# Kernel tuning notes

Measured on AMD Instinct MI355X. Metric: run time of the kernel, lower is better.

## Reference

```python
import jax, jax.numpy as jnp
import numpy as np

DN = ('NCHW', 'OIHW', 'NCHW')
LN_EPS = 1e-5
L2_EPS = 1e-12


def dwconv(x, w, pad):
    # depthwise conv: x [b,c,h,w], w [c,1,kh,kw]
    return jax.lax.conv_general_dilated(
        x, w, (1, 1), [(pad, pad), (pad, pad)],
        dimension_numbers=DN, feature_group_count=x.shape[1])


def l2norm(x):
    n = jnp.sqrt(jnp.sum(x * x, axis=-1, keepdims=True))
    return x / jnp.maximum(n, L2_EPS)


def setup_inputs() -> dict:
    key = jax.random.key(0)
    L, c, heads, mult = 2, 512, 8, 4
    cm = c * mult
    ks = jax.random.split(key, 18)
    rn = lambda k, s, sc=0.02: jax.random.normal(k, s, jnp.float32) * sc
    return {
        'x': jax.random.normal(ks[0], (2, c, 128, 128), jnp.float32),
        'Wq': rn(ks[1], (L, c, c)),
        'Wk': rn(ks[2], (L, c, c)),
        'Wv': rn(ks[3], (L, c, c)),
        'rescale': jnp.ones((L, heads, 1, 1), jnp.float32),
        'proj_W': rn(ks[4], (L, c, c)),
        'proj_b': jnp.zeros((L, c), jnp.float32),
        'pos_w1': rn(ks[5], (L, c, 1, 3, 3)),
        'pos_w2': rn(ks[6], (L, c, 1, 3, 3)),
        'ln_g': jnp.ones((L, c), jnp.float32),
        'ln_b': jnp.zeros((L, c), jnp.float32),
        'w1': rn(ks[7], (L, cm, c)),
        'dw1': rn(ks[8], (L, cm // 4, 1, 1, 1), 0.1),
        'dw3': rn(ks[9], (L, cm // 4, 1, 3, 3), 0.1),
        'dw5': rn(ks[10], (L, cm // 4, 1, 5, 5), 0.1),
        'dw7': rn(ks[11], (L, cm // 4, 1, 7, 7), 0.1),
        'w2': rn(ks[12], (L, c, cm)),
    }


def reference(x, Wq, Wk, Wv, rescale, proj_W, proj_b, pos_w1, pos_w2,
              ln_g, ln_b, w1, dw1, dw3, dw5, dw7, w2):
    b, c, H, W = x.shape
    heads = rescale.shape[1]
    d = c // heads
    n = H * W
    x = x.transpose(0, 2, 3, 1)  # [b,H,W,c]
    for l in range(Wq.shape[0]):
        # ---- S_MSA (channel-wise transposed attention) ----
        xf = x.reshape(b, n, c)
        q_inp = xf @ Wq[l]
        k_inp = xf @ Wk[l]
        v_inp = xf @ Wv[l]
        # [b,n,heads,d] -> [b,heads,d,n]
        to_hd = lambda t: t.reshape(b, n, heads, d).transpose(0, 2, 3, 1)
        q, k, v = to_hd(q_inp), to_hd(k_inp), to_hd(v_inp)
        q = l2norm(q)
        k = l2norm(k)
        attn = jnp.einsum('bhdn,bhen->bhde', k, q) * rescale[l]  # [b,h,d,d]
        attn = jax.nn.softmax(attn, axis=-1)
        o = jnp.einsum('bhde,bhen->bhdn', attn, v)
        o = o.transpose(0, 3, 1, 2).reshape(b, n, c)  # [b,n,heads*d]
        out_c = (o @ proj_W[l] + proj_b[l]).reshape(b, H, W, c)
        # positional branch on v_inp
        vimg = v_inp.reshape(b, H, W, c).transpose(0, 3, 1, 2)
        p = dwconv(vimg, pos_w1[l], 1)
        p = jax.nn.gelu(p, approximate=False)
        p = dwconv(p, pos_w2[l], 1)
        x = x + out_c + p.transpose(0, 2, 3, 1)
        # ---- PreNorm + MS_FFN ----
        mu = x.mean(-1, keepdims=True)
        var = jnp.mean((x - mu) ** 2, axis=-1, keepdims=True)
        xn = (x - mu) / jnp.sqrt(var + LN_EPS) * ln_g[l] + ln_b[l]
        y = xn.transpose(0, 3, 1, 2)  # [b,c,H,W]
        y = jnp.einsum('oc,bchw->bohw', w1[l], y)  # [b,4c,H,W]
        y1, y2, y3, y4 = jnp.split(y, 4, axis=1)
        o1 = dwconv(y1, dw1[l], 0)
        o2 = dwconv(y2, dw3[l], 1)
        o3 = dwconv(y3, dw5[l], 2)
        o4 = dwconv(y4, dw7[l], 3)
        o = jnp.concatenate([o1, o2, o3, o4], axis=1) + y
        o = jnp.einsum('oc,bchw->bohw', w2[l], o)  # [b,c,H,W]
        x = x + o.transpose(0, 2, 3, 1)
    return x.transpose(0, 3, 1, 2)
```

## Files before the change

### kernel.cpp

```cpp
#include <hip/hip_runtime.h>
#include <math.h>

typedef unsigned short u16;
typedef short bf16x8 __attribute__((ext_vector_type(8)));
typedef float f32x4 __attribute__((ext_vector_type(4)));
typedef float f32x2 __attribute__((ext_vector_type(2)));

__device__ __forceinline__ float bf2f(u16 h) {
    union { unsigned u; float f; } v; v.u = ((unsigned)h) << 16; return v.f;
}
__device__ __forceinline__ u16 f2bf(float f) {
    union { float f; unsigned u; } v; v.f = f;
    unsigned r = v.u + 0x7fffu + ((v.u >> 16) & 1u);
    return (u16)(r >> 16);
}
__device__ __forceinline__ f32x2 up2(unsigned u) {
    union { unsigned v; float f; } lo, hi;
    lo.v = u << 16; hi.v = u & 0xffff0000u;
    f32x2 r; r.x = lo.f; r.y = hi.f; return r;
}
__device__ __forceinline__ f32x2 unpk(unsigned u) { return up2(u); }
__device__ __forceinline__ f32x4 unpk(uint2 u) {
    f32x2 a = up2(u.x), b = up2(u.y);
    f32x4 r; r.x = a.x; r.y = a.y; r.z = b.x; r.w = b.y; return r;
}
__device__ __forceinline__ unsigned pkbf(f32x2 v) {
    return (unsigned)f2bf(v.x) | ((unsigned)f2bf(v.y) << 16);
}
__device__ __forceinline__ uint2 pkbf(f32x4 v) {
    uint2 r;
    r.x = (unsigned)f2bf(v.x) | ((unsigned)f2bf(v.y) << 16);
    r.y = (unsigned)f2bf(v.z) | ((unsigned)f2bf(v.w) << 16);
    return r;
}
__device__ __forceinline__ float gl(float v) {
    return 0.5f * v * (1.f + erff(v * 0.70710678118654752f));
}

__device__ __forceinline__ void gload_lds16(const u16* g, u16* l) {
    __builtin_amdgcn_global_load_lds(
        (const __attribute__((address_space(1))) void*)g,
        (__attribute__((address_space(3))) void*)l, 16, 0, 0);
}

template<int N> struct VecT;
template<> struct VecT<2> { typedef f32x2 T; typedef unsigned U; };
template<> struct VecT<4> { typedef f32x4 T; typedef uint2 U; };

#define CH    512
#define NPIX  16384
#define PTOT  32768
#define NHEAD 8

__global__ void transpose_k(const float* __restrict__ in, float* outF, u16* outB,
                            int R, int Cc, size_t ibs, size_t obs)
{
    __shared__ float tile[32][33];
    int z = blockIdx.z;
    const float* ip = in + (size_t)z * ibs;
    int c0 = blockIdx.x * 32, r0 = blockIdx.y * 32;
    int tx = threadIdx.x, ty = threadIdx.y;
#pragma unroll
    for (int j = 0; j < 4; j++)
        tile[ty + j * 8][tx] = ip[(size_t)(r0 + ty + j * 8) * Cc + c0 + tx];
    __syncthreads();
#pragma unroll
    for (int j = 0; j < 4; j++) {
        int orow = c0 + ty + j * 8, ocol = r0 + tx;
        float v = tile[tx][ty + j * 8];
        size_t o = (size_t)z * obs + (size_t)orow * R + ocol;
        if (outF) outF[o] = v;
        if (outB) outB[o] = f2bf(v);
    }
}

__global__ void transpose16_k(const u16* __restrict__ in, u16* __restrict__ out,
                              int R, int Cc, size_t ibs, size_t obs)
{
    __shared__ u16 tile[32][34];
    int z = blockIdx.z;
    const u16* ip = in + (size_t)z * ibs;
    int c0 = blockIdx.x * 32, r0 = blockIdx.y * 32;
    int tx = threadIdx.x, ty = threadIdx.y;
#pragma unroll
    for (int j = 0; j < 4; j++)
        tile[ty + j * 8][tx] = ip[(size_t)(r0 + ty + j * 8) * Cc + c0 + tx];
    __syncthreads();
#pragma unroll
    for (int j = 0; j < 4; j++)
        out[(size_t)z * obs + (size_t)(c0 + ty + j * 8) * R + r0 + tx] = tile[tx][ty + j * 8];
}

__global__ void cvt_bf16_k(const float* __restrict__ in, u16* __restrict__ out)
{
    size_t i = ((size_t)blockIdx.x * 256 + threadIdx.x) * 4;
    float4 v = *(const float4*)&in[i];
    uint2 st;
    st.x = (unsigned)f2bf(v.x) | ((unsigned)f2bf(v.y) << 16);
    st.y = (unsigned)f2bf(v.z) | ((unsigned)f2bf(v.w) << 16);
    *(uint2*)&out[i] = st;
}

__global__ void cvtw2_k(const float* __restrict__ in, const float* __restrict__ dw1,
                        u16* __restrict__ out)
{
    size_t i = ((size_t)blockIdx.x * 256 + threadIdx.x) * 4;
    int cp = (int)(i & 2047);
    int l = (int)(i >> 20);
    int src; bool ps = false;
    if (cp < 512)       src = 1024 + cp;
    else if (cp < 1024) src = 1536 + (cp - 512);
    else if (cp < 1536) { src = cp - 1024; ps = true; }
    else                src = 512 + (cp - 1536);
    float4 v = *(const float4*)&in[(i & ~(size_t)2047) + src];
    if (ps) {
        v.x *= 1.f + dw1[l * 512 + src];
        v.y *= 1.f + dw1[l * 512 + src + 1];
        v.z *= 1.f + dw1[l * 512 + src + 2];
        v.w *= 1.f + dw1[l * 512 + src + 3];
    }
    uint2 st;
    st.x = (unsigned)f2bf(v.x) | ((unsigned)f2bf(v.y) << 16);
    st.y = (unsigned)f2bf(v.z) | ((unsigned)f2bf(v.w) << 16);
    *(uint2*)&out[i] = st;
}

__global__ __launch_bounds__(512) void gemm5_k(
    const u16* __restrict__ A, const u16* __restrict__ Bw,
    int K, int ldb, int Nn, int rowsPerBatch, int bStride, int kChunk,
    const float* __restrict__ bias, const float* resid,
    float* outF, u16* outB, const u16* __restrict__ addB)
{
    __shared__ __attribute__((aligned(16))) u16 smem[6 * 4096];
    u16* Asb = smem;
    u16* Bsb = smem + 3 * 4096;
    int tid = threadIdx.x;

    int gx = gridDim.x;
    int nwg = gx * gridDim.y;
    int lin = blockIdx.y * gx + blockIdx.x;
    int swz = lin;
    if ((nwg & 7) == 0) swz = (lin & 7) * (nwg >> 3) + (lin >> 3);
    int bx = swz % gx, by = swz / gx;

    int rowBase = by * 128, colBase = bx * 128;
    const u16* Bp = Bw + (size_t)(rowBase / rowsPerBatch) * bStride;

    int kb = 0, ke = K;
    float* outFp = outF;
    if (kChunk) {
        kb = blockIdx.z * kChunk; ke = kb + kChunk;
        outFp = outF + (size_t)blockIdx.z * (size_t)gridDim.y * 128 * Nn;
    }

    f32x4 acc[4][2] = {};
    int lane = tid & 63, wave = tid >> 6;
    int wr = wave >> 2, wc = wave & 3;
    int lm = lane & 15, lk = lane >> 4;

    int row0 = tid >> 2;
    int kc   = ((tid ^ (tid >> 3)) & 3) * 8;
    int lb0  = (tid & ~63) * 8;

    const size_t aR0 = (size_t)(rowBase + row0) * K;
    const size_t bR0 = (size_t)(colBase + row0) * ldb;

    auto STAGE = [&](int bsel, int k0) {
        gload_lds16(&A [aR0 + k0 + kc], Asb + bsel * 4096 + lb0);
        gload_lds16(&Bp[bR0 + k0 + kc], Bsb + bsel * 4096 + lb0);
    };

    const int nsteps = (ke - kb) >> 5;
    STAGE(0, kb);
    STAGE(1, kb + 32);
    const int sl = (lk ^ ((lm >> 1) & 3)) * 8;

    for (int s = 0; s < nsteps; ++s) {
        asm volatile("s_waitcnt vmcnt(2)" ::: "memory");
        __builtin_amdgcn_s_barrier();
        __builtin_amdgcn_sched_barrier(0);
        int kpf = kb + ((s + 2 < nsteps) ? (s + 2) : (nsteps - 1)) * 32;
        STAGE((s + 2) % 3, kpf);

        const u16* Ab = Asb + (s % 3) * 4096;
        const u16* Bb = Bsb + (s % 3) * 4096;
        bf16x8 af[4], bfr[2];
#pragma unroll
        for (int mt = 0; mt < 4; mt++)
            af[mt] = *(const bf16x8*)&Ab[(wr * 64 + mt * 16 + lm) * 32 + sl];
#pragma unroll
        for (int nt = 0; nt < 2; nt++)
            bfr[nt] = *(const bf16x8*)&Bb[(wc * 32 + nt * 16 + lm) * 32 + sl];
        __builtin_amdgcn_s_setprio(1);
#pragma unroll
        for (int mt = 0; mt < 4; mt++)
#pragma unroll
            for (int nt = 0; nt < 2; nt++)
                acc[mt][nt] = __builtin_amdgcn_mfma_f32_16x16x32_bf16(
                    af[mt], bfr[nt], acc[mt][nt], 0, 0, 0);
        __builtin_amdgcn_s_setprio(0);
    }

    {
        float* smf = (float*)smem;
        constexpr int PADW = 132;
        const int erow = tid >> 5;
        const int ecol = (tid & 31) * 4;
        const int gcol = colBase + ecol;
        f32x4 bv = {};
        if (bias) {
            bv.x = bias[gcol];     bv.y = bias[gcol + 1];
            bv.z = bias[gcol + 2]; bv.w = bias[gcol + 3];
        }
        for (int hf = 0; hf < 4; ++hf) {
            if (hf == 0) {
                __syncthreads();
            } else {
                asm volatile("s_waitcnt lgkmcnt(0)" ::: "memory");
                __builtin_amdgcn_s_barrier();
            }
            if (wr == (hf >> 1)) {
                int mtb = (hf & 1) * 2;
#pragma unroll
                for (int m2 = 0; m2 < 2; m2++) {
#pragma unroll
                    for (int nt = 0; nt < 2; nt++) {
                        int lr = m2 * 16 + lk * 4;
                        int lc = wc * 32 + nt * 16 + lm;
#pragma unroll
                        for (int r = 0; r < 4; r++)
                            smf[(lr + r) * PADW + lc] = acc[mtb + m2][nt][r];
                    }
                }
            }
            int r0 = rowBase + hf * 32 + erow, r1 = r0 + 16;
            size_t o0 = (size_t)r0 * Nn + gcol, o1 = (size_t)r1 * Nn + gcol;
            f32x4 rv0 = {}, rv1 = {};
            uint2 av0 = {}, av1 = {};
            if (resid) { rv0 = *(const f32x4*)&resid[o0]; rv1 = *(const f32x4*)&resid[o1]; }
            if (addB)  { av0 = *(const uint2*)&addB[o0];  av1 = *(const uint2*)&addB[o1]; }
            asm volatile("s_waitcnt lgkmcnt(0)" ::: "memory");
            __builtin_amdgcn_s_barrier();
            f32x4 v0 = *(f32x4*)&smf[erow * PADW + ecol];
            f32x4 v1 = *(f32x4*)&smf[(erow + 16) * PADW + ecol];
            v0 += bv; v1 += bv;
            if (resid) { v0 += rv0; v1 += rv1; }
            if (addB)  { v0 += unpk(av0); v1 += unpk(av1); }
            if (outFp) { *(f32x4*)&outFp[o0] = v0; *(f32x4*)&outFp[o1] = v1; }
            if (outB) {
                uint2 p0 = pkbf(v0), p1 = pkbf(v1);
                *(uint2*)&outB[o0] = p0; *(uint2*)&outB[o1] = p1;
            }
        }
    }
}

template<int TM, int TN>
__global__ __launch_bounds__(256) void gemm_nt_k(
    const u16* __restrict__ A, const u16* __restrict__ Bw,
    int K, int ldb, int Nn, int rowsPerBatch, int bStride, int kChunk,
    const float* __restrict__ bias, const float* resid,
    float* outF, u16* outB, const u16* __restrict__ addB)
{
    constexpr int MT = TM / 32;
    constexpr int NT = TN / 32;
    constexpr int ABUF = TM * 32;
    constexpr int BBUF = TN * 32;
    __shared__ __attribute__((aligned(16))) u16 smem[2 * ABUF + 2 * BBUF];
    u16* Asb = smem;
    u16* Bsb = smem + 2 * ABUF;
    int tid = threadIdx.x;

    int gx = gridDim.x;
    int nwg = gx * gridDim.y;
    int lin = blockIdx.y * gx + blockIdx.x;
    int swz = lin;
    if ((nwg & 7) == 0) swz = (lin & 7) * (nwg >> 3) + (lin >> 3);
    int bx = swz % gx, by = swz / gx;

    int rowBase = by * TM, colBase = bx * TN;
    const u16* Bp = Bw + (size_t)(rowBase / rowsPerBatch) * bStride;

    int kb = 0, ke = K;
    float* outFp = outF;
    if (kChunk) {
        kb = blockIdx.z * kChunk; ke = kb + kChunk;
        outFp = outF + (size_t)blockIdx.z * (size_t)gridDim.y * TM * Nn;
    }

    f32x4 acc[MT][NT] = {};
    int lane = tid & 63, wave = tid >> 6;
    int wr = wave >> 1, wc = wave & 1;
    int lm = lane & 15, lk = lane >> 4;

    int row0 = tid >> 2;
    int kc   = ((tid ^ (tid >> 3)) & 3) * 8;
    int lb0  = (tid & ~63) * 8;

    const size_t aR0 = (size_t)(rowBase + row0) * K;
    const size_t bR0 = (size_t)(colBase + row0) * ldb;
    const size_t aR1 = (size_t)(rowBase + 64 + row0) * K;
    const size_t bR1 = (size_t)(colBase + 64 + row0) * ldb;

    auto STAGE = [&](int bsel, int k0) {
        gload_lds16(&A [aR0 + k0 + kc], Asb + bsel * ABUF + lb0);
        gload_lds16(&Bp[bR0 + k0 + kc], Bsb + bsel * BBUF + lb0);
        if constexpr (TM == 128)
            gload_lds16(&A [aR1 + k0 + kc], Asb + bsel * ABUF + lb0 + 2048);
        if constexpr (TN == 128)
            gload_lds16(&Bp[bR1 + k0 + kc], Bsb + bsel * BBUF + lb0 + 2048);
    };

    STAGE(0, kb);
    __syncthreads();
    int buf = 0;
    const int sl = (lk ^ ((lm >> 1) & 3)) * 8;

    for (int k0 = kb; k0 < ke; k0 += 32) {
        if (k0 + 32 < ke) STAGE(buf ^ 1, k0 + 32);
        const u16* Ab = Asb + buf * ABUF;
        const u16* Bb = Bsb + buf * BBUF;
        bf16x8 af[MT], bfr[NT];
#pragma unroll
        for (int mt = 0; mt < MT; mt++)
            af[mt] = *(const bf16x8*)&Ab[(wr * (TM / 2) + mt * 16 + lm) * 32 + sl];
#pragma unroll
        for (int nt = 0; nt < NT; nt++)
            bfr[nt] = *(const bf16x8*)&Bb[(wc * (TN / 2) + nt * 16 + lm) * 32 + sl];
#pragma unroll
        for (int mt = 0; mt < MT; mt++)
#pragma unroll
            for (int nt = 0; nt < NT; nt++)
                acc[mt][nt] = __builtin_amdgcn_mfma_f32_16x16x32_bf16(
                    af[mt], bfr[nt], acc[mt][nt], 0, 0, 0);
        __syncthreads();
        buf ^= 1;
    }

    {
        float* smf = (float*)smem;
        constexpr int PADW = TN + 4;
        constexpr int HALVES = TM / 32;
        constexpr int HPW = (MT / 2 > 0) ? MT / 2 : 1;
        const int erow = tid >> 5;
        const int ecol = (tid & 31) * 4;
        for (int hf = 0; hf < HALVES; ++hf) {
            __syncthreads();
            if (wr == hf / HPW) {
                int mtb = (hf % HPW) * 2;
#pragma unroll
                for (int m2 = 0; m2 < 2; m2++) {
#pragma unroll
                    for (int nt = 0; nt < NT; nt++) {
                        int lr = m2 * 16 + lk * 4;
                        int lc = wc * (TN / 2) + nt * 16 + lm;
#pragma unroll
                        for (int r = 0; r < 4; r++)
                            smf[(lr + r) * PADW + lc] = acc[mtb + m2][nt][r];
                    }
                }
            }
            __syncthreads();
#pragma unroll
            for (int p = 0; p < 4; p++) {
                int lrow = erow + p * 8;
                int grow = rowBase + hf * 32 + lrow;
                int gcol = colBase + ecol;
                f32x4 v = *(f32x4*)&smf[lrow * PADW + ecol];
                if (bias) {
                    v.x += bias[gcol];     v.y += bias[gcol + 1];
                    v.z += bias[gcol + 2]; v.w += bias[gcol + 3];
                }
                size_t o = (size_t)grow * Nn + gcol;
                if (resid) { f32x4 rv = *(const f32x4*)&resid[o]; v += rv; }
                if (addB)  { f32x4 av = unpk(*(const uint2*)&addB[o]); v += av; }
                if (outFp) *(f32x4*)&outFp[o] = v;
                if (outB) { uint2 pk = pkbf(v); *(uint2*)&outB[o] = pk; }
            }
        }
    }
}

__global__ void sreduce_k(const float* __restrict__ Sp, u16* __restrict__ Sbf)
{
    int i = blockIdx.x * 256 + threadIdx.x;
    float s = 0.f;
#pragma unroll
    for (int z = 0; z < 16; z++) s += Sp[(size_t)z * 524288 + i];
    Sbf[i] = f2bf(s);
}

__global__ void nrm_k(const float* __restrict__ Wqf, const float* __restrict__ Wkf,
                      const float* __restrict__ T12f,
                      float* __restrict__ QNI, float* __restrict__ KNI)
{
    int idx = blockIdx.x * 256 + threadIdx.x;
    int e = idx & 511, b = (idx >> 9) & 1, which = idx >> 10;
    const float* w = which ? Wkf : Wqf;
    const float* Tf = T12f + which * 512;
    float s = 0.f;
    for (int c = 0; c < 512; c++)
        s += w[c * 512 + e] * Tf[(size_t)(b * 512 + c) * 1024 + e];
    s = fmaxf(s, 0.f);
    float* outp = which ? KNI : QNI;
    outp[b * 512 + e] = 1.f / fmaxf(sqrtf(s), 1e-12f);
}

__global__ __launch_bounds__(256) void gsmall_k(
    const float* __restrict__ T2f, const float* __restrict__ Wq,
    const float* __restrict__ qinv, const float* __restrict__ kinv,
    const float* __restrict__ resc, float* __restrict__ att)
{
    __shared__ float t2l[64][64], wql[64][64];
    int t = threadIdx.x, h = blockIdx.x, b = blockIdx.y;
    const int eg = (t & 15) * 4;
    const int dg = (t >> 4) * 4;
    f32x4 acc[4] = {};
    for (int c0 = 0; c0 < 512; c0 += 64) {
        __syncthreads();
        for (int i = t; i < 4096; i += 256) {
            int cc = i >> 6, j = i & 63;
            t2l[cc][j] = T2f[(size_t)(b * 512 + c0 + cc) * 1024 + h * 64 + j];
            wql[cc][j] = Wq[(size_t)(c0 + cc) * 512 + h * 64 + j];
        }
        __syncthreads();
        for (int cc = 0; cc < 64; cc++) {
            f32x4 qv = *(f32x4*)&wql[cc][eg];
            f32x4 dv = *(f32x4*)&t2l[cc][dg];
            acc[0] += dv.x * qv;
            acc[1] += dv.y * qv;
            acc[2] += dv.z * qv;
            acc[3] += dv.w * qv;
        }
    }
    float rs = resc[h];
    f32x4 qn = *(const f32x4*)&qinv[b * 512 + h * 64 + eg];
    float* ap = att + (size_t)(b * 8 + h) * 4096;
#pragma unroll
    for (int dj = 0; dj < 4; dj++) {
        int d = dg + dj;
        float kn = kinv[b * 512 + h * 64 + d];
        f32x4 v = acc[dj] * kn;
        v = v * qn;
        v.x *= rs; v.y *= rs; v.z *= rs; v.w *= rs;
        float m = fmaxf(fmaxf(v.x, v.y), fmaxf(v.z, v.w));
        for (int off = 1; off <= 8; off <<= 1) m = fmaxf(m, __shfl_xor(m, off));
        f32x4 ev;
        ev.x = expf(v.x - m); ev.y = expf(v.y - m);
        ev.z = expf(v.z - m); ev.w = expf(v.w - m);
        float s = ev.x + ev.y + ev.z + ev.w;
        for (int off = 1; off <= 8; off <<= 1) s += __shfl_xor(s, off);
        f32x4 r;
        r.x = ev.x / s; r.y = ev.y / s; r.z = ev.z / s; r.w = ev.w / s;
        *(f32x4*)&ap[d * 64 + eg] = r;
    }
}

__global__ __launch_bounds__(256) void mbuild_k(const float* __restrict__ attn,
                                                const float* __restrict__ projW,
                                                u16* Mnt)
{
    __shared__ float at[64][64];
    __shared__ float pw[64][64];
    int t = threadIdx.x;
    int h = blockIdx.x, b = blockIdx.y, ot = blockIdx.z;
    const float* ap = attn + (size_t)(b * NHEAD + h) * 4096;
    for (int i = t; i < 4096; i += 256) {
        at[i >> 6][i & 63] = ap[i];
        pw[i >> 6][i & 63] = projW[(size_t)(h * 64 + (i >> 6)) * CH + ot * 64 + (i & 63)];
    }
    __syncthreads();
    const int eg = (t & 15) * 4;
    const int rg = (t >> 4) * 4;
    f32x4 acc[4] = {};
    for (int dd = 0; dd < 64; dd++) {
        f32x4 av = *(f32x4*)&at[dd][eg];
        f32x4 pv = *(f32x4*)&pw[dd][rg];
        acc[0] += pv.x * av;
        acc[1] += pv.y * av;
        acc[2] += pv.z * av;
        acc[3] += pv.w * av;
    }
#pragma unroll
    for (int j = 0; j < 4; j++) {
        uint2 pk = pkbf(acc[j]);
        *(uint2*)&Mnt[(size_t)b * (CH * CH)
                      + (size_t)(ot * 64 + rg + j) * CH + h * 64 + eg] = pk;
    }
}

template<int KS, int YS, int CPT, bool GELU_F, bool RESID, bool ACC, int SI, int SO>
__global__ __launch_bounds__(256, 1) void dwreg_k(
    const u16* __restrict__ in, const float* __restrict__ w,
    u16* __restrict__ outB, float* __restrict__ outAdd)
{
    constexpr int PAD = KS / 2;
    typedef typename VecT<CPT>::T fv;
    typedef typename VecT<CPT>::U uv;
    const int tid = threadIdx.x;
    const int cbase = (CPT == 4) ? ((tid & 127) * 4) : (tid * 2);
    const int x     = (CPT == 4) ? ((int)blockIdx.x * 2 + (tid >> 7)) : (int)blockIdx.x;
    const int y0 = blockIdx.y * YS;
    const int b  = blockIdx.z;
    const size_t bi = (size_t)b * NPIX * SI + cbase;
    const size_t bo = (size_t)b * NPIX * SO + cbase;

    fv wv[KS * KS];
#pragma unroll
    for (int t = 0; t < KS * KS; t++) {
        fv vv;
        vv.x = w[(cbase + 0) * KS * KS + t];
        vv.y = w[(cbase + 1) * KS * KS + t];
        if constexpr (CPT == 4) {
            vv.z = w[(cbase + 2) * KS * KS + t];
            vv.w = w[(cbase + 3) * KS * KS + t];
        }
        wv[t] = vv;
    }

    fv win[KS][KS];
    uv tmp[KS];

    auto rowload = [&](int t) {
        int yy = y0 - PAD + t;
        bool rv = ((unsigned)yy < 128u);
#pragma unroll
        for (int kx = 0; kx < KS; kx++) {
            int xx = x + kx - PAD;
            uv u = {};
            if (rv && ((unsigned)xx < 128u))
                u = *(const uv*)&in[bi + ((size_t)yy * 128 + xx) * SI];
            tmp[kx] = u;
        }
    };
    auto unpackrow = [&](int slot) {
#pragma unroll
        for (int kx = 0; kx < KS; kx++) win[slot][kx] = unpk(tmp[kx]);
    };

#pragma unroll
    for (int t = 0; t < KS - 1; t++) { rowload(t); unpackrow(t); }
    rowload(KS - 1);

    for (int i0 = 0; i0 < YS; i0 += KS) {
#pragma unroll
        for (int j = 0; j < KS; j++) {
            int i = i0 + j;
            if (i >= YS) break;
            unpackrow((j + KS - 1) % KS);
            if (i < YS - 1) rowload(i + KS);
            fv r = {};
#pragma unroll
            for (int ky = 0; ky < KS; ky++)
#pragma unroll
                for (int kx = 0; kx < KS; kx++)
                    r += win[(j + ky) % KS][kx] * wv[ky * KS + kx];
            if (GELU_F) {
                r.x = gl(r.x); r.y = gl(r.y);
                if constexpr (CPT == 4) { r.z = gl(r.z); r.w = gl(r.w); }
            }
            if (RESID) r += win[(j + PAD) % KS][PAD];
            size_t opos = bo + ((size_t)(y0 + i) * 128 + x) * SO;
            if (ACC) {
                fv* p = (fv*)&outAdd[opos];
                *p = *p + r;
            } else {
                uv pk = pkbf(r);
                *(uv*)&outB[opos] = pk;
            }
        }
    }
}

__global__ void ln_k(const float* __restrict__ xf, const float* __restrict__ g,
                     const float* __restrict__ bb, u16* __restrict__ xn)
{
    int t = threadIdx.x, lane = t & 63, wv = t >> 6;
    size_t pix = (size_t)blockIdx.x * 4 + wv;
    const float* row = xf + pix * CH;
    float4 a = *(const float4*)&row[lane * 8];
    float4 c = *(const float4*)&row[lane * 8 + 4];
    float s = a.x + a.y + a.z + a.w + c.x + c.y + c.z + c.w;
    float sq = a.x * a.x + a.y * a.y + a.z * a.z + a.w * a.w
             + c.x * c.x + c.y * c.y + c.z * c.z + c.w * c.w;
    for (int off = 32; off; off >>= 1) {
        s  += __shfl_xor(s, off);
        sq += __shfl_xor(sq, off);
    }
    float mu = s * (1.f / 512.f);
    float var = fmaxf(sq * (1.f / 512.f) - mu * mu, 0.f);
    float inv = rsqrtf(var + 1e-5f);
    float vals[8] = {a.x, a.y, a.z, a.w, c.x, c.y, c.z, c.w};
    unsigned o[4];
#pragma unroll
    for (int j = 0; j < 4; j++) {
        int cix = lane * 8 + j * 2;
        float v0 = (vals[j * 2] - mu) * inv * g[cix] + bb[cix];
        float v1 = (vals[j * 2 + 1] - mu) * inv * g[cix + 1] + bb[cix + 1];
        o[j] = (unsigned)f2bf(v0) | ((unsigned)f2bf(v1) << 16);
    }
    *(uint4*)&xn[pix * CH + lane * 8] = make_uint4(o[0], o[1], o[2], o[3]);
}

extern "C" void kernel_launch(void* const* d_in, const int* in_sizes, int n_in,
                              void* d_out, int out_size, void* d_ws, size_t ws_size,
                              hipStream_t stream)
{
    (void)in_sizes; (void)n_in; (void)out_size; (void)ws_size;
    const float* x_in  = (const float*)d_in[0];
    const float* Wq    = (const float*)d_in[1];
    const float* Wk    = (const float*)d_in[2];
    const float* Wv    = (const float*)d_in[3];
    const float* resc  = (const float*)d_in[4];
    const float* projW = (const float*)d_in[5];
    const float* projB = (const float*)d_in[6];
    const float* posw1 = (const float*)d_in[7];
    const float* posw2 = (const float*)d_in[8];
    const float* lng   = (const float*)d_in[9];
    const float* lnb   = (const float*)d_in[10];
    const float* w1    = (const float*)d_in[11];
    const float* dw1   = (const float*)d_in[12];
    const float* dw3   = (const float*)d_in[13];
    const float* dw5   = (const float*)d_in[14];
    const float* dw7   = (const float*)d_in[15];
    const float* w2    = (const float*)d_in[16];
    float* out = (float*)d_out;
    char* ws = (char*)d_ws;

    float* XF  = (float*)(ws + 0);
    u16*   XBb = (u16*)  (ws + 67108864ull);
    u16*   WQK = (u16*)  (ws + 100663296ull);
    u16*   WVt = (u16*)  (ws + 102760448ull);
    u16*   W1b = (u16*)  (ws + 103809024ull);
    u16*   W2b = (u16*)  (ws + 108003328ull);
    u16*   Mnt = (u16*)  (ws + 112197632ull);
    u16*   Sbf = (u16*)  (ws + 113246208ull);
    float* QNI = (float*)(ws + 118489088ull);
    float* KNI = (float*)(ws + 118493184ull);
    float* ATT = (float*)(ws + 118497280ull);

    u16*   R2  = (u16*)d_out;
    u16*   R3  = (u16*)d_out + 16777216;
    float* Sp  = (float*)((char*)d_out + 33554432ull);
    float* T12f= (float*)((char*)d_out + 33554432ull);
    u16*   Y2  = (u16*)d_out;

    const int BIG = 1 << 30;
    dim3 tb(32, 8);

    transpose_k<<<dim3(512, 16, 2), tb, 0, stream>>>(x_in, XF, XBb, 512, 16384, 8388608, 8388608);
    transpose_k<<<dim3(16, 16, 2), tb, 0, stream>>>(Wq, nullptr, WQK, 512, 512, 262144, 524288);
    transpose_k<<<dim3(16, 16, 2), tb, 0, stream>>>(Wk, nullptr, WQK + 262144, 512, 512, 262144, 524288);
    transpose_k<<<dim3(16, 16, 2), tb, 0, stream>>>(Wv, nullptr, WVt, 512, 512, 262144, 262144);
    cvt_bf16_k<<<2048, 256, 0, stream>>>(w1, W1b);
    cvtw2_k<<<2048, 256, 0, stream>>>(w2, dw1, W2b);

    for (int l = 0; l < 2; l++) {
        if (l == 0)
            cvt_bf16_k<<<16384, 256, 0, stream>>>(x_in, R2);
        else
            transpose16_k<<<dim3(16, 512, 2), tb, 0, stream>>>(XBb, R2, 16384, 512, 8388608, 8388608);
        gemm5_k<<<dim3(4, 8, 16), 512, 0, stream>>>(R2, R2, 16384, 16384, 512,
            512, 8388608, 1024, nullptr, nullptr, Sp, nullptr, nullptr);
        sreduce_k<<<2048, 256, 0, stream>>>(Sp, Sbf);
        gemm_nt_k<64, 128><<<dim3(8, 16), 256, 0, stream>>>(Sbf, WQK + l * 524288,
            512, 512, 1024, BIG, 0, 0, nullptr, nullptr, T12f, nullptr, nullptr);
        nrm_k<<<8, 256, 0, stream>>>(Wq + l * 262144, Wk + l * 262144, T12f, QNI, KNI);
        gsmall_k<<<dim3(8, 2), 256, 0, stream>>>(T12f + 512, Wq + l * 262144, QNI, KNI,
            resc + l * 8, ATT);
        mbuild_k<<<dim3(8, 2, 8), 256, 0, stream>>>(ATT, projW + l * 262144, Mnt);
        gemm5_k<<<dim3(4, 256), 512, 0, stream>>>(XBb, WVt + l * 262144, 512, 512, 512,
            BIG, 0, 0, nullptr, nullptr, nullptr, R3, nullptr);
        dwreg_k<3, 16, 4, true, false, false, 512, 512><<<dim3(64, 8, 2), 256, 0, stream>>>(
            R3, posw1 + l * 4608, R2, nullptr);
        dwreg_k<3, 16, 4, false, false, false, 512, 512><<<dim3(64, 8, 2), 256, 0, stream>>>(
            R2, posw2 + l * 4608, XBb, nullptr);
        gemm5_k<<<dim3(4, 256), 512, 0, stream>>>(R3, Mnt, 512, 512, 512,
            16384, 262144, 0, projB + l * 512, XF, XF, nullptr, XBb);
        ln_k<<<8192, 256, 0, stream>>>(XF, lng + l * 512, lnb + l * 512, XBb);
        for (int b2 = 0; b2 < 2; b2++) {
            const size_t boff = (size_t)b2 * NPIX * 512;
            const u16* w1l = W1b + l * 1048576;
            gemm5_k<<<dim3(8, 128), 512, 0, stream>>>(XBb + boff,
                w1l + 2 * 262144, 512, 512, 2048,
                BIG, 0, 0, nullptr, nullptr, nullptr, Y2 + 1024, nullptr);
            dwreg_k<5, 16, 2, false, true, false, 2048, 2048><<<dim3(128, 8, 1), 256, 0, stream>>>(
                Y2 + 1024, dw5 + l * 12800, Y2 + 0, nullptr);
            dwreg_k<7, 32, 2, false, true, false, 2048, 2048><<<dim3(128, 4, 1), 256, 0, stream>>>(
                Y2 + 1536, dw7 + l * 25088, Y2 + 512, nullptr);
            gemm5_k<<<dim3(4, 128), 512, 0, stream>>>(XBb + boff,
                w1l + 1 * 262144, 512, 512, 2048,
                BIG, 0, 0, nullptr, nullptr, nullptr, Y2 + 1024, nullptr);
            dwreg_k<3, 16, 4, false, true, false, 2048, 2048><<<dim3(64, 8, 1), 256, 0, stream>>>(
                Y2 + 1024, dw3 + l * 4608, Y2 + 1536, nullptr);
            gemm5_k<<<dim3(4, 128), 512, 0, stream>>>(XBb + boff,
                w1l + 0 * 262144, 512, 512, 2048,
                BIG, 0, 0, nullptr, nullptr, nullptr, Y2 + 1024, nullptr);
            gemm5_k<<<dim3(4, 128), 512, 0, stream>>>(Y2,
                W2b + l * 1048576, 2048, 2048, 512,
                BIG, 0, 0, nullptr, XF + boff, XF + boff, XBb + boff, nullptr);
        }
    }
    transpose_k<<<dim3(16, 512, 2), tb, 0, stream>>>(XF, out, nullptr, 16384, 512, 8388608, 8388608);
}
```

Before: 1.404 ms.

## Fold 1x1 FFN branch into w2 weights and skip symmetric Gram tiles

The 1x1 depthwise branch (group 0) is precomputed algebraically: w2_g0·diag(1+dw1)·w1_g0 is folded into a combined weight that multiplies xn directly, which removes one 512-wide w1 GEMM per batch. xn is copied into a slot of the Y2 buffer so the w2 GEMM handles it. The Gram matrix GEMM (X^T X) skips lower-triangle tiles, and the reduction kernel reads the mirrored entries. The w1 GEMMs for the other groups are merged into one wider launch. The trade-offs are an extra copy kernel, a weight-precompute GEMM, and a folded weight with different bf16 rounding.

```diff
diff --git a/kernel.cpp b/kernel.cpp
--- a/kernel.cpp
+++ b/kernel.cpp
@@ -101,35 +101,51 @@
     *(uint2*)&out[i] = st;
 }
 
-__global__ void cvtw2_k(const float* __restrict__ in, const float* __restrict__ dw1,
-                        u16* __restrict__ out)
+__global__ void cvtw2_k(const float* __restrict__ in, u16* __restrict__ out)
+{
+    size_t t = (size_t)blockIdx.x * 256 + threadIdx.x;
+    size_t i = t * 4;
+    int l  = (int)(i / 786432);
+    int rem = (int)(i - (size_t)l * 786432);
+    int o  = rem / 1536;
+    int cp = rem - o * 1536;
+    float4 v = *(const float4*)&in[(size_t)l * 1048576 + (size_t)o * 2048 + 512 + cp];
+    uint2 st;
+    st.x = (unsigned)f2bf(v.x) | ((unsigned)f2bf(v.y) << 16);
+    st.y = (unsigned)f2bf(v.z) | ((unsigned)f2bf(v.w) << 16);
+    *(uint2*)&out[(size_t)l * 1048576 + (size_t)o * 2048 + cp] = st;
+}
+
+__global__ void cvtw2g0_k(const float* __restrict__ w2, const float* __restrict__ dw1,
+                          u16* __restrict__ out)
 {
     size_t i = ((size_t)blockIdx.x * 256 + threadIdx.x) * 4;
-    int cp = (int)(i & 2047);
-    int l = (int)(i >> 20);
-    int src; bool ps = false;
-    if (cp < 512)       src = 1024 + cp;
-    else if (cp < 1024) src = 1536 + (cp - 512);
-    else if (cp < 1536) { src = cp - 1024; ps = true; }
-    else                src = 512 + (cp - 1536);
-    float4 v = *(const float4*)&in[(i & ~(size_t)2047) + src];
-    if (ps) {
-        v.x *= 1.f + dw1[l * 512 + src];
-        v.y *= 1.f + dw1[l * 512 + src + 1];
-        v.z *= 1.f + dw1[l * 512 + src + 2];
-        v.w *= 1.f + dw1[l * 512 + src + 3];
-    }
+    int c = (int)(i & 511);
+    int o = (int)((i >> 9) & 511);
+    int l = (int)(i >> 18);
+    float4 v = *(const float4*)&w2[(size_t)l * 1048576 + (size_t)o * 2048 + c];
+    v.x *= 1.f + dw1[l * 512 + c];
+    v.y *= 1.f + dw1[l * 512 + c + 1];
+    v.z *= 1.f + dw1[l * 512 + c + 2];
+    v.w *= 1.f + dw1[l * 512 + c + 3];
     uint2 st;
     st.x = (unsigned)f2bf(v.x) | ((unsigned)f2bf(v.y) << 16);
     st.y = (unsigned)f2bf(v.z) | ((unsigned)f2bf(v.w) << 16);
     *(uint2*)&out[i] = st;
 }
 
+__global__ void xcopy_k(const u16* __restrict__ in, u16* __restrict__ out)
+{
+    size_t i = ((size_t)blockIdx.x * 256 + threadIdx.x) * 8;
+    int row = (int)(i >> 9), col = (int)(i & 511);
+    *(uint4*)&out[(size_t)row * 2048 + 1536 + col] = *(const uint4*)&in[i];
+}
+
 __global__ __launch_bounds__(512) void gemm5_k(
     const u16* __restrict__ A, const u16* __restrict__ Bw,
     int K, int ldb, int Nn, int rowsPerBatch, int bStride, int kChunk,
     const float* __restrict__ bias, const float* resid,
-    float* outF, u16* outB, const u16* __restrict__ addB)
+    float* outF, u16* outB, const u16* __restrict__ addB, int symTri)
 {
     __shared__ __attribute__((aligned(16))) u16 smem[6 * 4096];
     u16* Asb = smem;
@@ -142,6 +158,8 @@
     int swz = lin;
     if ((nwg & 7) == 0) swz = (lin & 7) * (nwg >> 3) + (lin >> 3);
     int bx = swz % gx, by = swz / gx;
+
+    if (symTri && bx < (by & 3)) return;
 
     int rowBase = by * 128, colBase = bx * 128;
     const u16* Bp = Bw + (size_t)(rowBase / rowsPerBatch) * bStride;
@@ -384,9 +402,11 @@
 __global__ void sreduce_k(const float* __restrict__ Sp, u16* __restrict__ Sbf)
 {
     int i = blockIdx.x * 256 + threadIdx.x;
+    int b = i >> 18, rc = i & 262143, r = rc >> 9, c = rc & 511;
+    size_t src = (r > c) ? ((size_t)b << 18) + ((size_t)c << 9) + r : (size_t)i;
     float s = 0.f;
 #pragma unroll
-    for (int z = 0; z < 16; z++) s += Sp[(size_t)z * 524288 + i];
+    for (int z = 0; z < 16; z++) s += Sp[(size_t)z * 524288 + src];
     Sbf[i] = f2bf(s);
 }
 
@@ -644,6 +664,8 @@
     float* Sp  = (float*)((char*)d_out + 33554432ull);
     float* T12f= (float*)((char*)d_out + 33554432ull);
     u16*   Y2  = (u16*)d_out;
+    u16*   W2g0ps = (u16*)((char*)d_out + 50331648ull);
+    u16*   W1g0T  = (u16*)((char*)d_out + 51380224ull);
 
     const int BIG = 1 << 30;
     dim3 tb(32, 8);
@@ -653,7 +675,13 @@
     transpose_k<<<dim3(16, 16, 2), tb, 0, stream>>>(Wk, nullptr, WQK + 262144, 512, 512, 262144, 524288);
     transpose_k<<<dim3(16, 16, 2), tb, 0, stream>>>(Wv, nullptr, WVt, 512, 512, 262144, 262144);
     cvt_bf16_k<<<2048, 256, 0, stream>>>(w1, W1b);
-    cvtw2_k<<<2048, 256, 0, stream>>>(w2, dw1, W2b);
+    cvtw2_k<<<1536, 256, 0, stream>>>(w2, W2b);
+    cvtw2g0_k<<<512, 256, 0, stream>>>(w2, dw1, W2g0ps);
+    transpose_k<<<dim3(16, 16, 2), tb, 0, stream>>>(w1, nullptr, W1g0T, 512, 512, 1048576, 262144);
+    for (int l = 0; l < 2; l++)
+        gemm_nt_k<64, 128><<<dim3(4, 8), 256, 0, stream>>>(W2g0ps + l * 262144,
+            W1g0T + l * 262144, 512, 512, 2048, BIG, 0, 0,
+            nullptr, nullptr, nullptr, W2b + l * 1048576 + 1536, nullptr);
 
     for (int l = 0; l < 2; l++) {
         if (l == 0)
@@ -661,7 +689,7 @@
         else
             transpose16_k<<<dim3(16, 512, 2), tb, 0, stream>>>(XBb, R2, 16384, 512, 8388608, 8388608);
         gemm5_k<<<dim3(4, 8, 16), 512, 0, stream>>>(R2, R2, 16384, 16384, 512,
-            512, 8388608, 1024, nullptr, nullptr, Sp, nullptr, nullptr);
+            512, 8388608, 1024, nullptr, nullptr, Sp, nullptr, nullptr, 1);
         sreduce_k<<<2048, 256, 0, stream>>>(Sp, Sbf);
         gemm_nt_k<64, 128><<<dim3(8, 16), 256, 0, stream>>>(Sbf, WQK + l * 524288,
             512, 512, 1024, BIG, 0, 0, nullptr, nullptr, T12f, nullptr, nullptr);
@@ -670,35 +698,30 @@
             resc + l * 8, ATT);
         mbuild_k<<<dim3(8, 2, 8), 256, 0, stream>>>(ATT, projW + l * 262144, Mnt);
         gemm5_k<<<dim3(4, 256), 512, 0, stream>>>(XBb, WVt + l * 262144, 512, 512, 512,
-            BIG, 0, 0, nullptr, nullptr, nullptr, R3, nullptr);
+            BIG, 0, 0, nullptr, nullptr, nullptr, R3, nullptr, 0);
         dwreg_k<3, 16, 4, true, false, false, 512, 512><<<dim3(64, 8, 2), 256, 0, stream>>>(
             R3, posw1 + l * 4608, R2, nullptr);
         dwreg_k<3, 16, 4, false, false, false, 512, 512><<<dim3(64, 8, 2), 256, 0, stream>>>(
             R2, posw2 + l * 4608, XBb, nullptr);
         gemm5_k<<<dim3(4, 256), 512, 0, stream>>>(R3, Mnt, 512, 512, 512,
-            16384, 262144, 0, projB + l * 512, XF, XF, nullptr, XBb);
+            16384, 262144, 0, projB + l * 512, XF, XF, nullptr, XBb, 0);
         ln_k<<<8192, 256, 0, stream>>>(XF, lng + l * 512, lnb + l * 512, XBb);
         for (int b2 = 0; b2 < 2; b2++) {
             const size_t boff = (size_t)b2 * NPIX * 512;
             const u16* w1l = W1b + l * 1048576;
-            gemm5_k<<<dim3(8, 128), 512, 0, stream>>>(XBb + boff,
-                w1l + 2 * 262144, 512, 512, 2048,
-                BIG, 0, 0, nullptr, nullptr, nullptr, Y2 + 1024, nullptr);
+            gemm5_k<<<dim3(12, 128), 512, 0, stream>>>(XBb + boff,
+                w1l + 512 * 512, 512, 512, 2048,
+                BIG, 0, 0, nullptr, nullptr, nullptr, Y2 + 512, nullptr, 0);
+            dwreg_k<3, 16, 4, false, true, false, 2048, 2048><<<dim3(64, 8, 1), 256, 0, stream>>>(
+                Y2 + 512, dw3 + l * 4608, Y2 + 0, nullptr);
             dwreg_k<5, 16, 2, false, true, false, 2048, 2048><<<dim3(128, 8, 1), 256, 0, stream>>>(
-                Y2 + 1024, dw5 + l * 12800, Y2 + 0, nullptr);
+                Y2 + 1024, dw5 + l * 12800, Y2 + 512, nullptr);
             dwreg_k<7, 32, 2, false, true, false, 2048, 2048><<<dim3(128, 4, 1), 256, 0, stream>>>(
-                Y2 + 1536, dw7 + l * 25088, Y2 + 512, nullptr);
-            gemm5_k<<<dim3(4, 128), 512, 0, stream>>>(XBb + boff,
-                w1l + 1 * 262144, 512, 512, 2048,
-                BIG, 0, 0, nullptr, nullptr, nullptr, Y2 + 1024, nullptr);
-            dwreg_k<3, 16, 4, false, true, false, 2048, 2048><<<dim3(64, 8, 1), 256, 0, stream>>>(
-                Y2 + 1024, dw3 + l * 4608, Y2 + 1536, nullptr);
-            gemm5_k<<<dim3(4, 128), 512, 0, stream>>>(XBb + boff,
-                w1l + 0 * 262144, 512, 512, 2048,
-                BIG, 0, 0, nullptr, nullptr, nullptr, Y2 + 1024, nullptr);
+                Y2 + 1536, dw7 + l * 25088, Y2 + 1024, nullptr);
+            xcopy_k<<<4096, 256, 0, stream>>>(XBb + boff, Y2);
             gemm5_k<<<dim3(4, 128), 512, 0, stream>>>(Y2,
                 W2b + l * 1048576, 2048, 2048, 512,
-                BIG, 0, 0, nullptr, XF + boff, XF + boff, XBb + boff, nullptr);
+                BIG, 0, 0, nullptr, XF + boff, XF + boff, XBb + boff, nullptr, 0);
         }
     }
     transpose_k<<<dim3(16, 512, 2), tb, 0, stream>>>(XF, out, nullptr, 16384, 512, 8388608, 8388608);
```

Measured after the change: 1.415 ms. Within noise of the previous version (+0.8%).
